# Optimization experiments

Hardware: AMD Instinct MI355X
Metric: run time of the kernel (lower is better)

Reference implementation:

```python
import jax, jax.numpy as jnp
import numpy as np

DIM = 1024
NUM_HEADS = 16
NUM_KV_HEADS = 4
HEAD_DIM = 64
SOFT_CAP = 50.0
EPS = 1e-6


def setup_inputs() -> dict:
    key = jax.random.key(0)
    ks = jax.random.split(key, 8)
    B, T, S = 4, 128, 256
    q_dim = NUM_HEADS * HEAD_DIM
    kv_dim = NUM_KV_HEADS * HEAD_DIM
    s = 0.02
    return {
        "agent_tokens": jax.random.normal(ks[0], (B, T, DIM), jnp.float32),
        "z_tokens": jax.random.normal(ks[1], (B, T, S, DIM), jnp.float32),
        "Wq": jax.random.normal(ks[2], (DIM, q_dim), jnp.float32) * s,
        "Wk": jax.random.normal(ks[3], (DIM, kv_dim), jnp.float32) * s,
        "Wv": jax.random.normal(ks[4], (DIM, kv_dim), jnp.float32) * s,
        "Wo": jax.random.normal(ks[5], (q_dim, DIM), jnp.float32) * s,
        "q_gamma": 1.0 + jax.random.normal(ks[6], (HEAD_DIM,), jnp.float32) * s,
        "k_gamma": 1.0 + jax.random.normal(ks[7], (HEAD_DIM,), jnp.float32) * s,
    }


def _rmsnorm(x, gamma):
    # normalize over head_dim (last axis)
    var = jnp.mean(jnp.square(x), axis=-1, keepdims=True)
    return x * jax.lax.rsqrt(var + EPS) * gamma


def reference(agent_tokens, z_tokens, Wq, Wk, Wv, Wo, q_gamma, k_gamma):
    B, T, D = agent_tokens.shape
    S = z_tokens.shape[2]
    H, Hkv, hd = NUM_HEADS, NUM_KV_HEADS, HEAD_DIM
    G = H // Hkv
    scale = hd ** -0.5

    q = (agent_tokens @ Wq).reshape(B, T, H, hd)          # (B,T,H,hd)  single query per frame
    k = (z_tokens @ Wk).reshape(B, T, S, Hkv, hd)          # (B,T,S,Hkv,hd)
    v = (z_tokens @ Wv).reshape(B, T, S, Hkv, hd)

    q = _rmsnorm(q, q_gamma)
    k = _rmsnorm(k, k_gamma)

    # GQA: view q as (B,T,Hkv,G,hd) so each KV head serves G query heads
    qg = q.reshape(B, T, Hkv, G, hd)
    scores = jnp.einsum('btkgd,btskd->btkgs', qg, k) * scale   # (B,T,Hkv,G,S)
    scores = SOFT_CAP * jnp.tanh(scores / SOFT_CAP)
    attn = jax.nn.softmax(scores, axis=-1)
    out = jnp.einsum('btkgs,btskd->btkgd', attn, v)            # (B,T,Hkv,G,hd)
    out = out.reshape(B, T, H * hd)
    return out @ Wo                                            # (B,T,D)
```

## Files before the change

kernel.cpp:

```cpp
#include <hip/hip_runtime.h>
#include <hip/hip_bf16.h>

#define SOFTCAP_ 50.0f
#define EPS_ 1e-6f

typedef __attribute__((ext_vector_type(8))) short bf16x8;
typedef __attribute__((ext_vector_type(4))) float f32x4;

__device__ __forceinline__ unsigned short f2bf(float f) {
    unsigned u = __float_as_uint(f);
    u += 0x7FFFu + ((u >> 16) & 1u);
    return (unsigned short)(u >> 16);
}

__global__ void wkv_swizzle(const float* __restrict__ Wk, const float* __restrict__ Wv,
                            unsigned short* __restrict__ wkv) {
    int tid = blockIdx.x * 256 + threadIdx.x;
    int l = tid & 63;
    int nb = (tid >> 6) & 31;
    int kb = tid >> 11;
    int n = nb * 16 + (l & 15);
    int kbase = kb * 32 + ((l >> 4) << 3);
    const float* src = (n < 256) ? (Wk + n) : (Wv + (n - 256));
    unsigned short r[8];
#pragma unroll
    for (int j = 0; j < 8; ++j) r[j] = f2bf(src[(size_t)(kbase + j) * 256]);
    uint4 o;
    o.x = (unsigned)r[0] | ((unsigned)r[1] << 16);
    o.y = (unsigned)r[2] | ((unsigned)r[3] << 16);
    o.z = (unsigned)r[4] | ((unsigned)r[5] << 16);
    o.w = (unsigned)r[6] | ((unsigned)r[7] << 16);
    *(uint4*)(wkv + (size_t)tid * 8) = o;
}

__global__ __launch_bounds__(256) void qproj_kernel(
    const float* __restrict__ agent, const float* __restrict__ Wq,
    const float* __restrict__ q_gamma, float* __restrict__ ws_q)
{
    __shared__ float srows[8][1024];
    int cg = blockIdx.x, rg = blockIdx.y;
    int t = threadIdx.x;
#pragma unroll
    for (int j = 0; j < 8; ++j) {
        int f = j * 256 + t;
        int row = f >> 8, c4 = f & 255;
        *(float4*)&srows[row][c4 * 4] =
            *(const float4*)(agent + (size_t)(rg * 8 + row) * 1024 + c4 * 4);
    }
    __syncthreads();
    int c = cg * 64 + (t & 63);
    int rq = t >> 6;
    float acc0 = 0.f, acc1 = 0.f;
    for (int k = 0; k < 1024; k += 4) {
        float w0 = Wq[(size_t)(k + 0) * 1024 + c];
        float w1 = Wq[(size_t)(k + 1) * 1024 + c];
        float w2 = Wq[(size_t)(k + 2) * 1024 + c];
        float w3 = Wq[(size_t)(k + 3) * 1024 + c];
        float4 a0 = *(const float4*)&srows[rq * 2][k];
        float4 a1 = *(const float4*)&srows[rq * 2 + 1][k];
        acc0 += a0.x * w0 + a0.y * w1 + a0.z * w2 + a0.w * w3;
        acc1 += a1.x * w0 + a1.y * w1 + a1.z * w2 + a1.w * w3;
    }
    float g = q_gamma[t & 63];
    float ss0 = acc0 * acc0, ss1 = acc1 * acc1;
#pragma unroll
    for (int d = 1; d < 64; d <<= 1) { ss0 += __shfl_xor(ss0, d); ss1 += __shfl_xor(ss1, d); }
    float rs0 = rsqrtf(ss0 * (1.0f / 64.0f) + EPS_);
    float rs1 = rsqrtf(ss1 * (1.0f / 64.0f) + EPS_);
    ws_q[(size_t)(rg * 8 + rq * 2 + 0) * 1024 + c] = acc0 * rs0 * g;
    ws_q[(size_t)(rg * 8 + rq * 2 + 1) * 1024 + c] = acc1 * rs1 * g;
}

__global__ __launch_bounds__(512, 4) void kv_attn_kernel(
    const float* __restrict__ z, const unsigned short* __restrict__ wkv,
    const float* __restrict__ ws_q, const float* __restrict__ k_gamma,
    float* __restrict__ ws_att)
{
    __shared__ __align__(16) unsigned short zlds[32 * 256];
    __shared__ float p_lds[16 * 32];
    __shared__ float den_lds[16];
    const int bt = blockIdx.x;
    const int tid = threadIdx.x;
    const int w = tid >> 6;
    const bool isK = (w < 4);
    const int kvh = w & 3;
    const int nbase = isK ? (kvh * 4) : (16 + kvh * 4);
    const int l = tid & 63, l15 = l & 15, lg = l >> 4;

    float qn[4][4], kgm[4];
    if (isK) {
#pragma unroll
        for (int g = 0; g < 4; ++g)
#pragma unroll
            for (int ni = 0; ni < 4; ++ni)
                qn[g][ni] = ws_q[(size_t)bt * 1024 + (kvh * 4 + g) * 64 + ni * 16 + l15];
#pragma unroll
        for (int ni = 0; ni < 4; ++ni) kgm[ni] = k_gamma[ni * 16 + l15];
    }

    float out_acc[4][4] = {};
    float denom[4] = {};

    for (int sc = 0; sc < 8; ++sc) {
        f32x4 acc[2][4];
#pragma unroll
        for (int mi = 0; mi < 2; ++mi)
#pragma unroll
            for (int ni = 0; ni < 4; ++ni) acc[mi][ni] = (f32x4){0.f, 0.f, 0.f, 0.f};

        for (int sl = 0; sl < 4; ++sl) {
            __syncthreads();
#pragma unroll
            for (int j = 0; j < 4; ++j) {
                int f = j * 512 + tid;
                int row = f >> 6, c4 = f & 63;
                float4 v4 = *(const float4*)(z + (size_t)(bt * 256 + sc * 32 + row) * 1024
                                               + sl * 256 + c4 * 4);
                unsigned lo = (unsigned)f2bf(v4.x) | ((unsigned)f2bf(v4.y) << 16);
                unsigned hi = (unsigned)f2bf(v4.z) | ((unsigned)f2bf(v4.w) << 16);
                int byteoff = ((row * 512) + c4 * 8) ^ ((row & 7) << 4);
                *(uint2*)((char*)zlds + byteoff) = (uint2){lo, hi};
            }
            __syncthreads();
#pragma unroll
            for (int ksl = 0; ksl < 8; ++ksl) {
                const int kb = sl * 8 + ksl;
                int boff0 = ((l15 * 512) + ksl * 64 + lg * 16) ^ ((l15 & 7) << 4);
                bf16x8 a0 = *(const bf16x8*)((const char*)zlds + boff0);
                bf16x8 a1 = *(const bf16x8*)((const char*)zlds + boff0 + 8192);
                bf16x8 b[4];
#pragma unroll
                for (int ni = 0; ni < 4; ++ni)
                    b[ni] = *(const bf16x8*)(wkv + ((size_t)(kb * 32 + nbase + ni) * 64 + l) * 8);
#pragma unroll
                for (int ni = 0; ni < 4; ++ni) {
                    acc[0][ni] = __builtin_amdgcn_mfma_f32_16x16x32_bf16(a0, b[ni], acc[0][ni], 0, 0, 0);
                    acc[1][ni] = __builtin_amdgcn_mfma_f32_16x16x32_bf16(a1, b[ni], acc[1][ni], 0, 0, 0);
                }
            }
        }
        if (isK) {
#pragma unroll
            for (int mi = 0; mi < 2; ++mi) {
#pragma unroll
                for (int r = 0; r < 4; ++r) {
                    float k0 = acc[mi][0][r], k1 = acc[mi][1][r], k2 = acc[mi][2][r], k3 = acc[mi][3][r];
                    float ss = k0 * k0 + k1 * k1 + k2 * k2 + k3 * k3;
                    ss += __shfl_xor(ss, 1); ss += __shfl_xor(ss, 2);
                    ss += __shfl_xor(ss, 4); ss += __shfl_xor(ss, 8);
                    float rs = rsqrtf(ss * (1.0f / 64.0f) + EPS_);
                    k0 *= rs * kgm[0]; k1 *= rs * kgm[1]; k2 *= rs * kgm[2]; k3 *= rs * kgm[3];
#pragma unroll
                    for (int g = 0; g < 4; ++g) {
                        float sp = qn[g][0] * k0 + qn[g][1] * k1 + qn[g][2] * k2 + qn[g][3] * k3;
                        sp += __shfl_xor(sp, 1); sp += __shfl_xor(sp, 2);
                        sp += __shfl_xor(sp, 4); sp += __shfl_xor(sp, 8);
                        float scv = sp * 0.125f;
                        float e2 = __expf(scv * (2.0f / SOFTCAP_));
                        float th = 1.0f - 2.0f / (e2 + 1.0f);
                        float p = __expf(SOFTCAP_ * th);
                        denom[g] += p;
                        if (l15 == g)
                            p_lds[(kvh * 4 + g) * 32 + mi * 16 + lg * 4 + r] = p;
                    }
                }
            }
        }
        __syncthreads();
        if (!isK) {
#pragma unroll
            for (int mi = 0; mi < 2; ++mi)
#pragma unroll
                for (int r = 0; r < 4; ++r) {
                    int row = mi * 16 + lg * 4 + r;
#pragma unroll
                    for (int g = 0; g < 4; ++g) {
                        float p = p_lds[(kvh * 4 + g) * 32 + row];
                        out_acc[g][0] += p * acc[mi][0][r];
                        out_acc[g][1] += p * acc[mi][1][r];
                        out_acc[g][2] += p * acc[mi][2][r];
                        out_acc[g][3] += p * acc[mi][3][r];
                    }
                }
        }
    }
    if (isK) {
#pragma unroll
        for (int g = 0; g < 4; ++g) {
            float d = denom[g];
            d += __shfl_xor(d, 16); d += __shfl_xor(d, 32);
            if (l == g) den_lds[kvh * 4 + g] = d;
        }
    }
    __syncthreads();
    if (!isK) {
#pragma unroll
        for (int g = 0; g < 4; ++g) {
            float inv = 1.0f / den_lds[kvh * 4 + g];
#pragma unroll
            for (int ni = 0; ni < 4; ++ni) {
                float o = out_acc[g][ni];
                o += __shfl_xor(o, 16); o += __shfl_xor(o, 32);
                if (lg == 0)
                    ws_att[(size_t)bt * 1024 + (kvh * 4 + g) * 64 + ni * 16 + l15] = o * inv;
            }
        }
    }
}

__global__ __launch_bounds__(256) void oproj_kernel(
    const float* __restrict__ att, const float* __restrict__ Wo,
    float* __restrict__ out)
{
    __shared__ float srows[8][1024];
    int cg = blockIdx.x, rg = blockIdx.y;
    int t = threadIdx.x;
#pragma unroll
    for (int j = 0; j < 8; ++j) {
        int f = j * 256 + t;
        int row = f >> 8, c4 = f & 255;
        *(float4*)&srows[row][c4 * 4] =
            *(const float4*)(att + (size_t)(rg * 8 + row) * 1024 + c4 * 4);
    }
    __syncthreads();
    int c = cg * 64 + (t & 63);
    int rq = t >> 6;
    float acc0 = 0.f, acc1 = 0.f;
    for (int k = 0; k < 1024; k += 4) {
        float w0 = Wo[(size_t)(k + 0) * 1024 + c];
        float w1 = Wo[(size_t)(k + 1) * 1024 + c];
        float w2 = Wo[(size_t)(k + 2) * 1024 + c];
        float w3 = Wo[(size_t)(k + 3) * 1024 + c];
        float4 a0 = *(const float4*)&srows[rq * 2][k];
        float4 a1 = *(const float4*)&srows[rq * 2 + 1][k];
        acc0 += a0.x * w0 + a0.y * w1 + a0.z * w2 + a0.w * w3;
        acc1 += a1.x * w0 + a1.y * w1 + a1.z * w2 + a1.w * w3;
    }
    out[(size_t)(rg * 8 + rq * 2 + 0) * 1024 + c] = acc0;
    out[(size_t)(rg * 8 + rq * 2 + 1) * 1024 + c] = acc1;
}

extern "C" void kernel_launch(void* const* d_in, const int* in_sizes, int n_in,
                              void* d_out, int out_size, void* d_ws, size_t ws_size,
                              hipStream_t stream) {
    const float* agent = (const float*)d_in[0];
    const float* z     = (const float*)d_in[1];
    const float* Wq    = (const float*)d_in[2];
    const float* Wk    = (const float*)d_in[3];
    const float* Wv    = (const float*)d_in[4];
    const float* Wo    = (const float*)d_in[5];
    const float* qg    = (const float*)d_in[6];
    const float* kg    = (const float*)d_in[7];
    float* out = (float*)d_out;

    char* ws = (char*)d_ws;
    float* ws_q   = (float*)ws;
    float* ws_att = (float*)(ws + (2u << 20));
    unsigned short* ws_wkv = (unsigned short*)(ws + (4u << 20));

    hipLaunchKernelGGL(wkv_swizzle, dim3(256), dim3(256), 0, stream, Wk, Wv, ws_wkv);
    hipLaunchKernelGGL(qproj_kernel, dim3(16, 64), dim3(256), 0, stream, agent, Wq, qg, ws_q);
    hipLaunchKernelGGL(kv_attn_kernel, dim3(512), dim3(512), 0, stream, z, ws_wkv, ws_q, kg, ws_att);
    hipLaunchKernelGGL(oproj_kernel, dim3(16, 64), dim3(256), 0, stream, ws_att, Wo, out);
}
```

Before: 435.1 us.

## Reassociate attention as (P·z)·Wv to drop the per-token V projection

Instead of projecting every z row to V with MFMA and then weighting by the softmax probabilities, the kernel first forms a probability-weighted sum of raw z rows for each query head using bf16 MFMA. It then applies Wv once per frame with a scalar GEMV in a tail phase. This removes half of the per-token projection MFMA work, and whole z chunks are staged in a larger shared buffer with one pair of barriers per chunk. In exchange it uses about 66KB of LDS per block, which may lower occupancy, and the tail does strided scalar global reads of Wv in every block. Probabilities are also rounded to bf16.

```diff
diff --git a/kernel.cpp b/kernel.cpp
--- a/kernel.cpp
+++ b/kernel.cpp
@@ -74,72 +74,77 @@
 __global__ __launch_bounds__(512, 4) void kv_attn_kernel(
     const float* __restrict__ z, const unsigned short* __restrict__ wkv,
     const float* __restrict__ ws_q, const float* __restrict__ k_gamma,
-    float* __restrict__ ws_att)
+    const float* __restrict__ Wv, float* __restrict__ ws_att)
 {
-    __shared__ __align__(16) unsigned short zlds[32 * 256];
-    __shared__ float p_lds[16 * 32];
+    __shared__ __align__(16) char smem[65792];
+    __shared__ __align__(16) unsigned short p_lds[16][40];
     __shared__ float den_lds[16];
+    unsigned short* zlds = (unsigned short*)smem;
+    float* y_lds = (float*)smem;
     const int bt = blockIdx.x;
     const int tid = threadIdx.x;
     const int w = tid >> 6;
     const bool isK = (w < 4);
-    const int kvh = w & 3;
-    const int nbase = isK ? (kvh * 4) : (16 + kvh * 4);
+    const int h = w & 3;
     const int l = tid & 63, l15 = l & 15, lg = l >> 4;
 
     float qn[4][4], kgm[4];
+    float denom[4] = {};
     if (isK) {
 #pragma unroll
         for (int g = 0; g < 4; ++g)
 #pragma unroll
             for (int ni = 0; ni < 4; ++ni)
-                qn[g][ni] = ws_q[(size_t)bt * 1024 + (kvh * 4 + g) * 64 + ni * 16 + l15];
+                qn[g][ni] = ws_q[(size_t)bt * 1024 + (h * 4 + g) * 64 + ni * 16 + l15];
 #pragma unroll
         for (int ni = 0; ni < 4; ++ni) kgm[ni] = k_gamma[ni * 16 + l15];
     }
-
-    float out_acc[4][4] = {};
-    float denom[4] = {};
+    f32x4 Y[16];
+#pragma unroll
+    for (int t = 0; t < 16; ++t) Y[t] = (f32x4){0.f, 0.f, 0.f, 0.f};
 
     for (int sc = 0; sc < 8; ++sc) {
-        f32x4 acc[2][4];
-#pragma unroll
-        for (int mi = 0; mi < 2; ++mi)
-#pragma unroll
-            for (int ni = 0; ni < 4; ++ni) acc[mi][ni] = (f32x4){0.f, 0.f, 0.f, 0.f};
-
-        for (int sl = 0; sl < 4; ++sl) {
-            __syncthreads();
-#pragma unroll
-            for (int j = 0; j < 4; ++j) {
-                int f = j * 512 + tid;
-                int row = f >> 6, c4 = f & 63;
-                float4 v4 = *(const float4*)(z + (size_t)(bt * 256 + sc * 32 + row) * 1024
-                                               + sl * 256 + c4 * 4);
-                unsigned lo = (unsigned)f2bf(v4.x) | ((unsigned)f2bf(v4.y) << 16);
-                unsigned hi = (unsigned)f2bf(v4.z) | ((unsigned)f2bf(v4.w) << 16);
-                int byteoff = ((row * 512) + c4 * 8) ^ ((row & 7) << 4);
-                *(uint2*)((char*)zlds + byteoff) = (uint2){lo, hi};
-            }
-            __syncthreads();
-#pragma unroll
-            for (int ksl = 0; ksl < 8; ++ksl) {
-                const int kb = sl * 8 + ksl;
-                int boff0 = ((l15 * 512) + ksl * 64 + lg * 16) ^ ((l15 & 7) << 4);
-                bf16x8 a0 = *(const bf16x8*)((const char*)zlds + boff0);
-                bf16x8 a1 = *(const bf16x8*)((const char*)zlds + boff0 + 8192);
+        __syncthreads();
+#pragma unroll
+        for (int b = 0; b < 4; ++b) {
+            float4 v[4];
+#pragma unroll
+            for (int i = 0; i < 4; ++i) {
+                int f = (b * 4 + i) * 512 + tid;
+                int row = f >> 8, c4 = f & 255;
+                v[i] = *(const float4*)(z + (size_t)(bt * 256 + sc * 32 + row) * 1024 + c4 * 4);
+            }
+#pragma unroll
+            for (int i = 0; i < 4; ++i) {
+                int f = (b * 4 + i) * 512 + tid;
+                int row = f >> 8, c4 = f & 255;
+                unsigned lo = (unsigned)f2bf(v[i].x) | ((unsigned)f2bf(v[i].y) << 16);
+                unsigned hi = (unsigned)f2bf(v[i].z) | ((unsigned)f2bf(v[i].w) << 16);
+                int off = (row * 2048 + c4 * 8) ^ ((row & 7) << 4);
+                *(uint2*)(smem + off) = (uint2){lo, hi};
+            }
+        }
+        __syncthreads();
+        if (isK) {
+            f32x4 acc[2][4];
+#pragma unroll
+            for (int mi = 0; mi < 2; ++mi)
+#pragma unroll
+                for (int ni = 0; ni < 4; ++ni) acc[mi][ni] = (f32x4){0.f, 0.f, 0.f, 0.f};
+            for (int kb = 0; kb < 32; ++kb) {
+                int o0 = (l15 * 2048 + kb * 64 + lg * 16) ^ ((l15 & 7) << 4);
+                bf16x8 a0 = *(const bf16x8*)(smem + o0);
+                bf16x8 a1 = *(const bf16x8*)(smem + o0 + 32768);
                 bf16x8 b[4];
 #pragma unroll
                 for (int ni = 0; ni < 4; ++ni)
-                    b[ni] = *(const bf16x8*)(wkv + ((size_t)(kb * 32 + nbase + ni) * 64 + l) * 8);
+                    b[ni] = *(const bf16x8*)(wkv + ((size_t)(kb * 32 + h * 4 + ni) * 64 + l) * 8);
 #pragma unroll
                 for (int ni = 0; ni < 4; ++ni) {
                     acc[0][ni] = __builtin_amdgcn_mfma_f32_16x16x32_bf16(a0, b[ni], acc[0][ni], 0, 0, 0);
                     acc[1][ni] = __builtin_amdgcn_mfma_f32_16x16x32_bf16(a1, b[ni], acc[1][ni], 0, 0, 0);
                 }
             }
-        }
-        if (isK) {
 #pragma unroll
             for (int mi = 0; mi < 2; ++mi) {
 #pragma unroll
@@ -161,27 +166,28 @@
                         float p = __expf(SOFTCAP_ * th);
                         denom[g] += p;
                         if (l15 == g)
-                            p_lds[(kvh * 4 + g) * 32 + mi * 16 + lg * 4 + r] = p;
+                            p_lds[h * 4 + g][mi * 16 + lg * 4 + r] = f2bf(p);
                     }
                 }
             }
         }
         __syncthreads();
         if (!isK) {
-#pragma unroll
-            for (int mi = 0; mi < 2; ++mi)
-#pragma unroll
-                for (int r = 0; r < 4; ++r) {
-                    int row = mi * 16 + lg * 4 + r;
-#pragma unroll
-                    for (int g = 0; g < 4; ++g) {
-                        float p = p_lds[(kvh * 4 + g) * 32 + row];
-                        out_acc[g][0] += p * acc[mi][0][r];
-                        out_acc[g][1] += p * acc[mi][1][r];
-                        out_acc[g][2] += p * acc[mi][2][r];
-                        out_acc[g][3] += p * acc[mi][3][r];
-                    }
+            bf16x8 ap = *(const bf16x8*)((const char*)p_lds + l15 * 80 + lg * 16);
+#pragma unroll
+            for (int t = 0; t < 16; ++t) {
+                int c0 = h * 256 + t * 16;
+                unsigned short g8[8];
+#pragma unroll
+                for (int jj = 0; jj < 8; ++jj) {
+                    int s = lg * 8 + jj;
+                    int off = (s * 2048 + (c0 + l15) * 2) ^ (jj << 4);
+                    g8[jj] = *(const unsigned short*)(smem + off);
                 }
+                bf16x8 bz = {(short)g8[0], (short)g8[1], (short)g8[2], (short)g8[3],
+                             (short)g8[4], (short)g8[5], (short)g8[6], (short)g8[7]};
+                Y[t] = __builtin_amdgcn_mfma_f32_16x16x32_bf16(ap, bz, Y[t], 0, 0, 0);
+            }
         }
     }
     if (isK) {
@@ -189,22 +195,46 @@
         for (int g = 0; g < 4; ++g) {
             float d = denom[g];
             d += __shfl_xor(d, 16); d += __shfl_xor(d, 32);
-            if (l == g) den_lds[kvh * 4 + g] = d;
+            if (l == g) den_lds[h * 4 + g] = d;
         }
     }
     __syncthreads();
     if (!isK) {
 #pragma unroll
-        for (int g = 0; g < 4; ++g) {
-            float inv = 1.0f / den_lds[kvh * 4 + g];
-#pragma unroll
-            for (int ni = 0; ni < 4; ++ni) {
-                float o = out_acc[g][ni];
-                o += __shfl_xor(o, 16); o += __shfl_xor(o, 32);
-                if (lg == 0)
-                    ws_att[(size_t)bt * 1024 + (kvh * 4 + g) * 64 + ni * 16 + l15] = o * inv;
-            }
-        }
+        for (int t = 0; t < 16; ++t)
+#pragma unroll
+            for (int r = 0; r < 4; ++r)
+                y_lds[(lg * 4 + r) * 1028 + h * 256 + t * 16 + l15] = Y[t][r];
+    }
+    __syncthreads();
+    if (tid < 256) {
+        int cb = tid >> 6, d = tid & 63;
+        int col = cb * 64 + d;
+        float a0 = 0.f, a1 = 0.f, a2 = 0.f, a3 = 0.f;
+        const float* y0 = y_lds + (cb * 4 + 0) * 1028;
+        const float* y1 = y_lds + (cb * 4 + 1) * 1028;
+        const float* y2 = y_lds + (cb * 4 + 2) * 1028;
+        const float* y3 = y_lds + (cb * 4 + 3) * 1028;
+        for (int k = 0; k < 1024; k += 4) {
+            float4 wv;
+            wv.x = Wv[(size_t)(k + 0) * 256 + col];
+            wv.y = Wv[(size_t)(k + 1) * 256 + col];
+            wv.z = Wv[(size_t)(k + 2) * 256 + col];
+            wv.w = Wv[(size_t)(k + 3) * 256 + col];
+            float4 v0 = *(const float4*)(y0 + k);
+            float4 v1 = *(const float4*)(y1 + k);
+            float4 v2 = *(const float4*)(y2 + k);
+            float4 v3 = *(const float4*)(y3 + k);
+            a0 += v0.x * wv.x + v0.y * wv.y + v0.z * wv.z + v0.w * wv.w;
+            a1 += v1.x * wv.x + v1.y * wv.y + v1.z * wv.z + v1.w * wv.w;
+            a2 += v2.x * wv.x + v2.y * wv.y + v2.z * wv.z + v2.w * wv.w;
+            a3 += v3.x * wv.x + v3.y * wv.y + v3.z * wv.z + v3.w * wv.w;
+        }
+        float* outp = ws_att + (size_t)bt * 1024;
+        outp[(cb * 4 + 0) * 64 + d] = a0 / den_lds[cb * 4 + 0];
+        outp[(cb * 4 + 1) * 64 + d] = a1 / den_lds[cb * 4 + 1];
+        outp[(cb * 4 + 2) * 64 + d] = a2 / den_lds[cb * 4 + 2];
+        outp[(cb * 4 + 3) * 64 + d] = a3 / den_lds[cb * 4 + 3];
     }
 }
 
@@ -260,6 +290,6 @@
 
     hipLaunchKernelGGL(wkv_swizzle, dim3(256), dim3(256), 0, stream, Wk, Wv, ws_wkv);
     hipLaunchKernelGGL(qproj_kernel, dim3(16, 64), dim3(256), 0, stream, agent, Wq, qg, ws_q);
-    hipLaunchKernelGGL(kv_attn_kernel, dim3(512), dim3(512), 0, stream, z, ws_wkv, ws_q, kg, ws_att);
+    hipLaunchKernelGGL(kv_attn_kernel, dim3(512), dim3(512), 0, stream, z, ws_wkv, ws_q, kg, Wv, ws_att);
     hipLaunchKernelGGL(oproj_kernel, dim3(16, 64), dim3(256), 0, stream, ws_att, Wo, out);
 }
```

New measurement: 744.5 us. +71.1%, slower.
